# Optimization experiments

Hardware: AMD Instinct MI355X
Metric: run time of the kernel (lower is better)

## Reference

```python
import jax, jax.numpy as jnp
import numpy as np
import math

B, N, D, K = 4, 4096, 1024, 8


def setup_inputs() -> dict:
    key = jax.random.key(0)
    ks = jax.random.split(key, 9)
    s = 0.02
    return {
        "summaries": jax.random.normal(ks[0], (B, N, D), dtype=jnp.float32),
        "Wq": jax.random.normal(ks[1], (D, D), dtype=jnp.float32) * s,
        "bq": jnp.zeros((D,), dtype=jnp.float32),
        "Wk": jax.random.normal(ks[2], (D, D), dtype=jnp.float32) * s,
        "bk": jnp.zeros((D,), dtype=jnp.float32),
        "Wv": jax.random.normal(ks[3], (D, D), dtype=jnp.float32) * s,
        "bv": jnp.zeros((D,), dtype=jnp.float32),
        "Wo": jax.random.normal(ks[4], (D, D), dtype=jnp.float32) * s,
        "bo": jnp.zeros((D,), dtype=jnp.float32),
    }


def reference(summaries, Wq, bq, Wk, bk, Wv, bv, Wo, bo):
    b_, n_, d_ = summaries.shape
    q = summaries @ Wq + bq
    k = summaries @ Wk + bk
    v = summaries @ Wv + bv
    # [B, N, N] causal scores
    scores = jnp.einsum("bnd,bmd->bnm", q, k) / math.sqrt(d_)
    causal = jnp.triu(jnp.full((n_, n_), -jnp.inf, dtype=scores.dtype), k=1)
    scores = scores + causal
    # top-k sparse attention (N > K here, matching the torch branch)
    topk_vals, topk_idx = jax.lax.top_k(scores, K)  # [B, N, K]
    bi = jnp.arange(b_)[:, None, None]
    ri = jnp.arange(n_)[None, :, None]
    sparse = jnp.full_like(scores, -jnp.inf).at[bi, ri, topk_idx].set(topk_vals)
    attn = jax.nn.softmax(sparse, axis=-1)
    out = jnp.einsum("bnm,bmd->bnd", attn, v)
    return out @ Wo + bo
```

## Files before the change

### kernel.cpp

```cpp
#include <hip/hip_runtime.h>
#include <cstdint>
#include <cstddef>

#define B_ 4
#define N_ 4096
#define D_ 1024
#define CAND 16
#define M_ (B_*N_)
#define MD_ ((size_t)M_ * D_)
#define DD_ ((size_t)D_ * D_)

typedef __attribute__((ext_vector_type(8))) short short8;
typedef __attribute__((ext_vector_type(4))) float floatx4;

__device__ __align__(16) float          g_Qf[MD_];
__device__ __align__(16) float          g_Kf[MD_];
__device__ __align__(16) unsigned short g_Qb[MD_];
__device__ __align__(16) unsigned short g_Kb[MD_];
__device__ __align__(16) float          g_Vf[MD_];
__device__ __align__(16) unsigned short g_AO[MD_];
__device__ __align__(16) unsigned short g_X0[MD_];
__device__ __align__(16) unsigned short g_X1[MD_];
__device__ __align__(16) unsigned short g_Wq0T[DD_];
__device__ __align__(16) unsigned short g_Wq1T[DD_];
__device__ __align__(16) unsigned short g_Wk0T[DD_];
__device__ __align__(16) unsigned short g_Wk1T[DD_];
__device__ __align__(16) unsigned short g_WvT[DD_];
__device__ __align__(16) unsigned short g_WoT[DD_];
__device__ __align__(16) float          g_S[(size_t)B_ * N_ * N_];
__device__ __align__(16) int            g_cand[(size_t)M_ * CAND];
__device__ __align__(16) int            g_t8i[(size_t)M_ * 8];
__device__ __align__(16) float          g_t8w[(size_t)M_ * 8];

__device__ __forceinline__ float b2f(unsigned short u){
  return __uint_as_float(((unsigned int)u) << 16);
}
__device__ __forceinline__ unsigned short f2b(float f){
  unsigned int b = __float_as_uint(f);
  b += 0x7fffu + ((b >> 16) & 1u);
  return (unsigned short)(b >> 16);
}
__device__ __forceinline__ void split2(float x, unsigned short& h0,
                                       unsigned short& h1){
  h0 = f2b(x);
  float r1 = x - b2f(h0);
  h1 = f2b(r1);
}

__device__ __forceinline__ void gl_lds16(const void* g, void* l){
  __builtin_amdgcn_global_load_lds(
      (const __attribute__((address_space(1))) unsigned int*)g,
      (__attribute__((address_space(3))) unsigned int*)l, 16, 0, 0);
}

__global__ __launch_bounds__(256)
void transpose2(const float* __restrict__ Wv, const float* __restrict__ Wo){
  __shared__ float tile[32][33];
  const float* src = blockIdx.z ? Wo : Wv;
  unsigned short* dst = blockIdx.z ? g_WoT : g_WvT;
  int tx = threadIdx.x, ty = threadIdx.y;
  int n0 = blockIdx.x * 32, k0 = blockIdx.y * 32;
  for (int r = ty; r < 32; r += 8) tile[r][tx] = src[(size_t)(k0 + r) * D_ + n0 + tx];
  __syncthreads();
  for (int r = ty; r < 32; r += 8) dst[(size_t)(n0 + r) * D_ + k0 + tx] = f2b(tile[tx][r]);
}

__global__ __launch_bounds__(256)
void split_wT(const float* __restrict__ Wq, const float* __restrict__ Wk){
  __shared__ float tile[32][33];
  const float* src = blockIdx.z ? Wk : Wq;
  unsigned short* d0 = blockIdx.z ? g_Wk0T : g_Wq0T;
  unsigned short* d1 = blockIdx.z ? g_Wk1T : g_Wq1T;
  int tx = threadIdx.x, ty = threadIdx.y;
  int n0 = blockIdx.x * 32, k0 = blockIdx.y * 32;
  for (int r = ty; r < 32; r += 8) tile[r][tx] = src[(size_t)(k0 + r) * D_ + n0 + tx];
  __syncthreads();
  for (int r = ty; r < 32; r += 8){
    unsigned short h0, h1;
    split2(tile[tx][r], h0, h1);
    size_t o = (size_t)(n0 + r) * D_ + k0 + tx;
    d0[o] = h0; d1[o] = h1;
  }
}

__global__ __launch_bounds__(256)
void split_x(const float* __restrict__ X){
  size_t i = ((size_t)blockIdx.x * 256 + threadIdx.x) * 4;
  if (i >= MD_) return;
  float4 x = *(const float4*)&X[i];
  ushort4 u0, u1;
  split2(x.x, u0.x, u1.x);
  split2(x.y, u0.y, u1.y);
  split2(x.z, u0.z, u1.z);
  split2(x.w, u0.w, u1.w);
  *(ushort4*)&g_X0[i] = u0;
  *(ushort4*)&g_X1[i] = u1;
}

__global__ __launch_bounds__(256, 2)
void qk_split_gemm(const float* __restrict__ bq, const float* __restrict__ bk){
  int p = blockIdx.x;
  int lin = (p & 7) * 256 + (p >> 3);
  int mt = lin >> 4;
  int sub = lin & 15;
  int which = sub >> 3;
  int nt = sub & 7;

  const unsigned short* __restrict__ B0 = which ? g_Wk0T : g_Wq0T;
  const unsigned short* __restrict__ B1 = which ? g_Wk1T : g_Wq1T;
  const float* __restrict__ bias = which ? bk : bq;
  float* __restrict__ outf = which ? g_Kf : g_Qf;
  unsigned short* __restrict__ outb = which ? g_Kb : g_Qb;

  __shared__ unsigned short __align__(16) As[2][128 * 32];
  __shared__ unsigned short __align__(16) Bs[2][128 * 32];

  int tid = threadIdx.x;
  size_t m0 = (size_t)mt * 128;
  int n0 = nt * 128;
  int l = tid & 63, wid = tid >> 6;
  int wm = (wid >> 1) * 64, wn = (wid & 1) * 64;
  int quad = l >> 4, lr = l & 15;
  int srow = tid >> 2, scol = (tid & 3) * 8;

  floatx4 acc[4][4];
  #pragma unroll
  for (int i = 0; i < 4; i++)
    #pragma unroll
    for (int j = 0; j < 4; j++) acc[i][j] = (floatx4)0.0f;

  for (int k0 = 0; k0 < D_; k0 += 32){
    #pragma unroll
    for (int it2 = 0; it2 < 2; it2++){
      int r = srow + it2 * 64;
      size_t ao = (m0 + r) * D_ + k0 + scol;
      size_t bo = (size_t)(n0 + r) * D_ + k0 + scol;
      int so = r * 32 + scol;
      gl_lds16(&g_X0[ao], &As[0][so]);
      gl_lds16(&g_X1[ao], &As[1][so]);
      gl_lds16(&B0[bo], &Bs[0][so]);
      gl_lds16(&B1[bo], &Bs[1][so]);
    }
    __syncthreads();
    short8 a0[4], a1[4], b0[4], b1[4];
    #pragma unroll
    for (int i = 0; i < 4; i++){
      int ro = (wm + i * 16 + lr) * 32 + quad * 8;
      a0[i] = *(short8*)&As[0][ro];
      a1[i] = *(short8*)&As[1][ro];
    }
    #pragma unroll
    for (int j = 0; j < 4; j++){
      int ro = (wn + j * 16 + lr) * 32 + quad * 8;
      b0[j] = *(short8*)&Bs[0][ro];
      b1[j] = *(short8*)&Bs[1][ro];
    }
    #pragma unroll
    for (int i = 0; i < 4; i++)
      #pragma unroll
      for (int j = 0; j < 4; j++){
        acc[i][j] = __builtin_amdgcn_mfma_f32_16x16x32_bf16(a0[i], b1[j], acc[i][j], 0, 0, 0);
        acc[i][j] = __builtin_amdgcn_mfma_f32_16x16x32_bf16(a1[i], b0[j], acc[i][j], 0, 0, 0);
        acc[i][j] = __builtin_amdgcn_mfma_f32_16x16x32_bf16(a0[i], b0[j], acc[i][j], 0, 0, 0);
      }
    __syncthreads();
  }
  #pragma unroll
  for (int i = 0; i < 4; i++)
    #pragma unroll
    for (int j = 0; j < 4; j++)
      #pragma unroll
      for (int rg = 0; rg < 4; rg++){
        size_t row = m0 + wm + i * 16 + quad * 4 + rg;
        int col = n0 + wn + j * 16 + lr;
        float val = acc[i][j][rg] + bias[col];
        outf[row * D_ + col] = val;
        outb[row * D_ + col] = f2b(val);
      }
}

__global__ __launch_bounds__(256)
void gemm_bf16(const float* __restrict__ bias, float* __restrict__ Cout, int sel){
  const unsigned short* Asrc = sel ? g_AO : g_X0;
  const unsigned short* Bt = sel ? g_WoT : g_WvT;
  float* C = sel ? Cout : g_Vf;
  __shared__ unsigned short __align__(16) As[128 * 32];
  __shared__ unsigned short __align__(16) Bs[128 * 32];
  int p = blockIdx.x;
  int lin = (p & 7) * 128 + (p >> 3);
  int mt = lin >> 3;
  int nt = lin & 7;
  int tid = threadIdx.x;
  size_t m0 = (size_t)mt * 128;
  int n0 = nt * 128;
  int l = tid & 63, wid = tid >> 6;
  int wm = (wid >> 1) * 64, wn = (wid & 1) * 64;
  int quad = l >> 4, lr = l & 15;
  int srow = tid >> 2, scol = (tid & 3) * 8;
  floatx4 acc[4][4];
  #pragma unroll
  for (int i = 0; i < 4; i++)
    #pragma unroll
    for (int j = 0; j < 4; j++) acc[i][j] = (floatx4)0.0f;

  for (int k0 = 0; k0 < D_; k0 += 32){
    #pragma unroll
    for (int it = 0; it < 2; it++){
      int r = srow + it * 64;
      int so = r * 32 + scol;
      gl_lds16(&Asrc[(m0 + r) * D_ + k0 + scol], &As[so]);
      gl_lds16(&Bt[(size_t)(n0 + r) * D_ + k0 + scol], &Bs[so]);
    }
    __syncthreads();
    short8 af[4], bf[4];
    #pragma unroll
    for (int i = 0; i < 4; i++) af[i] = *(short8*)&As[(wm + i * 16 + lr) * 32 + quad * 8];
    #pragma unroll
    for (int j = 0; j < 4; j++) bf[j] = *(short8*)&Bs[(wn + j * 16 + lr) * 32 + quad * 8];
    #pragma unroll
    for (int i = 0; i < 4; i++)
      #pragma unroll
      for (int j = 0; j < 4; j++)
        acc[i][j] = __builtin_amdgcn_mfma_f32_16x16x32_bf16(af[i], bf[j], acc[i][j], 0, 0, 0);
    __syncthreads();
  }
  #pragma unroll
  for (int i = 0; i < 4; i++)
    #pragma unroll
    for (int j = 0; j < 4; j++)
      #pragma unroll
      for (int rg = 0; rg < 4; rg++){
        size_t row = m0 + wm + i * 16 + quad * 4 + rg;
        int col = n0 + wn + j * 16 + lr;
        C[row * D_ + col] = acc[i][j][rg] + bias[col];
      }
}

__global__ __launch_bounds__(256)
void scores_gemm(){
  int jt = blockIdx.x, it = blockIdx.y, b = blockIdx.z;
  if (jt > it) return;
  __shared__ unsigned short __align__(16) As[128 * 32];
  __shared__ unsigned short __align__(16) Bs[128 * 32];
  int tid = threadIdx.x;
  size_t am0 = (size_t)b * N_ + it * 128;
  size_t bn0 = (size_t)b * N_ + jt * 128;
  int l = tid & 63, wid = tid >> 6;
  int wm = (wid >> 1) * 64, wn = (wid & 1) * 64;
  int quad = l >> 4, lr = l & 15;
  int srow = tid >> 2, scol = (tid & 3) * 8;
  floatx4 acc[4][4];
  #pragma unroll
  for (int i = 0; i < 4; i++)
    #pragma unroll
    for (int j = 0; j < 4; j++) acc[i][j] = (floatx4)0.0f;

  for (int k0 = 0; k0 < D_; k0 += 32){
    #pragma unroll
    for (int it2 = 0; it2 < 2; it2++){
      int r = srow + it2 * 64;
      int so = r * 32 + scol;
      gl_lds16(&g_Qb[(am0 + r) * D_ + k0 + scol], &As[so]);
      gl_lds16(&g_Kb[(bn0 + r) * D_ + k0 + scol], &Bs[so]);
    }
    __syncthreads();
    short8 af[4], bf[4];
    #pragma unroll
    for (int i = 0; i < 4; i++) af[i] = *(short8*)&As[(wm + i * 16 + lr) * 32 + quad * 8];
    #pragma unroll
    for (int j = 0; j < 4; j++) bf[j] = *(short8*)&Bs[(wn + j * 16 + lr) * 32 + quad * 8];
    #pragma unroll
    for (int i = 0; i < 4; i++)
      #pragma unroll
      for (int j = 0; j < 4; j++)
        acc[i][j] = __builtin_amdgcn_mfma_f32_16x16x32_bf16(af[i], bf[j], acc[i][j], 0, 0, 0);
    __syncthreads();
  }
  #pragma unroll
  for (int i = 0; i < 4; i++)
    #pragma unroll
    for (int j = 0; j < 4; j++)
      #pragma unroll
      for (int rg = 0; rg < 4; rg++){
        int row = it * 128 + wm + i * 16 + quad * 4 + rg;
        int col = jt * 128 + wn + j * 16 + lr;
        float v = acc[i][j][rg] * 0.03125f;
        if (col > row) v = -3.0e38f;
        g_S[((size_t)b * N_ + row) * N_ + col] = v;
      }
}

__global__ __launch_bounds__(256)
void row_topk(){
  __shared__ float lv[CAND * 256];
  __shared__ int   li[CAND * 256];
  int w = threadIdx.x >> 6, l = threadIdx.x & 63;
  int g = threadIdx.x;
  int i = blockIdx.x * 4 + w;
  int irow = i & (N_ - 1);
  const float* Srow = &g_S[(size_t)i * N_];
  #pragma unroll
  for (int u = 0; u < CAND; u++){ lv[u * 256 + g] = -3.0e38f; li[u * 256 + g] = -1; }
  float vmin = -3.0e38f; int pmin = 0;
  for (int j0 = l * 4; j0 <= irow; j0 += 256){
    float4 v4 = *(const float4*)&Srow[j0];
    #pragma unroll
    for (int e = 0; e < 4; e++){
      float v = (&v4.x)[e];
      if (v > vmin){
        lv[pmin * 256 + g] = v; li[pmin * 256 + g] = j0 + e;
        float m = lv[g]; int p = 0;
        #pragma unroll
        for (int u = 1; u < CAND; u++){ float x = lv[u * 256 + g]; if (x < m){ m = x; p = u; } }
        vmin = m; pmin = p;
      }
    }
  }
  float mv = lv[g]; int mp = 0;
  #pragma unroll
  for (int u = 1; u < CAND; u++){ float x = lv[u * 256 + g]; if (x > mv){ mv = x; mp = u; } }
  int mj = li[mp * 256 + g];
  for (int rd = 0; rd < CAND; rd++){
    float bv = mv; int bj = mj; int bl = l;
    #pragma unroll
    for (int off = 32; off >= 1; off >>= 1){
      float ov = __shfl_xor(bv, off);
      int oj = __shfl_xor(bj, off);
      int ol = __shfl_xor(bl, off);
      if (ov > bv || (ov == bv && ol < bl)){ bv = ov; bj = oj; bl = ol; }
    }
    bool valid = (bv > -2.9e38f);
    if (l == 0) g_cand[(size_t)i * CAND + rd] = valid ? bj : -1;
    if (valid && bl == l){
      lv[mp * 256 + g] = -3.0e38f;
      mv = lv[g]; mp = 0;
      #pragma unroll
      for (int u = 1; u < CAND; u++){ float x = lv[u * 256 + g]; if (x > mv){ mv = x; mp = u; } }
      mj = li[mp * 256 + g];
    }
  }
}

__global__ __launch_bounds__(256)
void rescore_top8(){
  int i = blockIdx.x;
  int b = i >> 12;
  int tid = threadIdx.x, l = tid & 63, w = tid >> 6;
  __shared__ double cs[CAND];
  __shared__ int cid[CAND];
  if (tid < CAND) cid[tid] = g_cand[(size_t)i * CAND + tid];
  __syncthreads();
  double q[16];
  #pragma unroll
  for (int u = 0; u < 16; u++) q[u] = (double)g_Qf[(size_t)i * D_ + l + 64 * u];
  for (int c = w * 4; c < w * 4 + 4; c++){
    int j = cid[c];
    double s = 0.0;
    if (j >= 0){
      size_t ko = ((size_t)(b * N_ + j)) * D_;
      #pragma unroll
      for (int u = 0; u < 16; u++) s = fma(q[u], (double)g_Kf[ko + l + 64 * u], s);
    }
    #pragma unroll
    for (int off = 32; off >= 1; off >>= 1) s += __shfl_down(s, off);
    if (l == 0) cs[c] = (j >= 0) ? s * 0.03125 : -1.0e300;
  }
  __syncthreads();
  if (tid == 0){
    double v8[8]; int i8[8];
    bool used[CAND];
    for (int u = 0; u < CAND; u++) used[u] = false;
    for (int rk = 0; rk < 8; rk++){
      double best = -1.0e300; int bp = -1;
      for (int c = 0; c < CAND; c++)
        if (!used[c] && cid[c] >= 0 && cs[c] > best){ best = cs[c]; bp = c; }
      if (bp >= 0){ used[bp] = true; v8[rk] = best; i8[rk] = cid[bp]; }
      else { v8[rk] = -1.0e300; i8[rk] = -1; }
    }
    if (i8[0] < 0){ i8[0] = i & (N_ - 1); v8[0] = 0.0; }
    double mx = v8[0];
    double e[8]; double Z = 0.0;
    for (int rk = 0; rk < 8; rk++){
      e[rk] = (i8[rk] >= 0) ? exp(v8[rk] - mx) : 0.0;
      Z += e[rk];
    }
    for (int rk = 0; rk < 8; rk++){
      g_t8i[(size_t)i * 8 + rk] = i8[rk];
      g_t8w[(size_t)i * 8 + rk] = (float)(e[rk] / Z);
    }
  }
}

__global__ __launch_bounds__(256)
void gather_v(){
  int i = blockIdx.x;
  int b = i >> 12;
  int tid = threadIdx.x;
  __shared__ float ws8[8];
  __shared__ int id8[8];
  if (tid < 8){ ws8[tid] = g_t8w[(size_t)i * 8 + tid]; id8[tid] = g_t8i[(size_t)i * 8 + tid]; }
  __syncthreads();
  int d0 = tid * 4;
  float a0 = 0.f, a1 = 0.f, a2 = 0.f, a3 = 0.f;
  #pragma unroll
  for (int rk = 0; rk < 8; rk++){
    int j = id8[rk];
    if (j < 0) continue;
    float wgt = ws8[rk];
    float4 vv = *(const float4*)&g_Vf[((size_t)(b * N_ + j)) * D_ + d0];
    a0 += wgt * vv.x; a1 += wgt * vv.y; a2 += wgt * vv.z; a3 += wgt * vv.w;
  }
  ushort4 o;
  o.x = f2b(a0); o.y = f2b(a1); o.z = f2b(a2); o.w = f2b(a3);
  *(ushort4*)&g_AO[(size_t)i * D_ + d0] = o;
}

extern "C" void kernel_launch(void* const* d_in, const int* in_sizes, int n_in,
                              void* d_out, int out_size, void* d_ws, size_t ws_size,
                              hipStream_t stream){
  const float* S  = (const float*)d_in[0];
  const float* Wq = (const float*)d_in[1];
  const float* bq = (const float*)d_in[2];
  const float* Wk = (const float*)d_in[3];
  const float* bk = (const float*)d_in[4];
  const float* Wv = (const float*)d_in[5];
  const float* bv = (const float*)d_in[6];
  const float* Wo = (const float*)d_in[7];
  const float* bo = (const float*)d_in[8];
  float* out = (float*)d_out;
  (void)d_ws; (void)ws_size; (void)in_sizes; (void)n_in; (void)out_size;

  transpose2<<<dim3(32, 32, 2), dim3(32, 8), 0, stream>>>(Wv, Wo);
  split_wT<<<dim3(32, 32, 2), dim3(32, 8), 0, stream>>>(Wq, Wk);
  split_x<<<dim3(M_), 256, 0, stream>>>(S);
  qk_split_gemm<<<dim3(2048), 256, 0, stream>>>(bq, bk);
  gemm_bf16<<<dim3(1024), 256, 0, stream>>>(bv, nullptr, 0);
  scores_gemm<<<dim3(32, 32, 4), 256, 0, stream>>>();
  row_topk<<<dim3(M_ / 4), 256, 0, stream>>>();
  rescore_top8<<<dim3(M_), 256, 0, stream>>>();
  gather_v<<<dim3(M_), 256, 0, stream>>>();
  gemm_bf16<<<dim3(1024), 256, 0, stream>>>(bo, out, 1);
}
```

Before: 1.122 ms.

## Interleave split-bf16 hi/lo operands so Q/K GEMM runs as longer-K single GEMM

```diff
diff --git a/kernel.cpp b/kernel.cpp
--- a/kernel.cpp
+++ b/kernel.cpp
@@ -20,11 +20,11 @@
 __device__ __align__(16) float          g_Vf[MD_];
 __device__ __align__(16) unsigned short g_AO[MD_];
 __device__ __align__(16) unsigned short g_X0[MD_];
-__device__ __align__(16) unsigned short g_X1[MD_];
+__device__ __align__(16) unsigned short g_Xpk[2 * MD_];
 __device__ __align__(16) unsigned short g_Wq0T[DD_];
-__device__ __align__(16) unsigned short g_Wq1T[DD_];
 __device__ __align__(16) unsigned short g_Wk0T[DD_];
-__device__ __align__(16) unsigned short g_Wk1T[DD_];
+__device__ __align__(16) unsigned short g_Wqpk[2 * DD_];
+__device__ __align__(16) unsigned short g_Wkpk[2 * DD_];
 __device__ __align__(16) unsigned short g_WvT[DD_];
 __device__ __align__(16) unsigned short g_WoT[DD_];
 __device__ __align__(16) float          g_S[(size_t)B_ * N_ * N_];
@@ -69,8 +69,8 @@
 void split_wT(const float* __restrict__ Wq, const float* __restrict__ Wk){
   __shared__ float tile[32][33];
   const float* src = blockIdx.z ? Wk : Wq;
-  unsigned short* d0 = blockIdx.z ? g_Wk0T : g_Wq0T;
-  unsigned short* d1 = blockIdx.z ? g_Wk1T : g_Wq1T;
+  unsigned short* d0  = blockIdx.z ? g_Wk0T : g_Wq0T;
+  unsigned short* dpk = blockIdx.z ? g_Wkpk : g_Wqpk;
   int tx = threadIdx.x, ty = threadIdx.y;
   int n0 = blockIdx.x * 32, k0 = blockIdx.y * 32;
   for (int r = ty; r < 32; r += 8) tile[r][tx] = src[(size_t)(k0 + r) * D_ + n0 + tx];
@@ -79,7 +79,9 @@
     unsigned short h0, h1;
     split2(tile[tx][r], h0, h1);
     size_t o = (size_t)(n0 + r) * D_ + k0 + tx;
-    d0[o] = h0; d1[o] = h1;
+    d0[o] = h0;
+    *(unsigned int*)&dpk[(size_t)(n0 + r) * (2 * D_) + 2 * (k0 + tx)] =
+        (unsigned int)h1 | ((unsigned int)h0 << 16);
   }
 }
 
@@ -88,17 +90,19 @@
   size_t i = ((size_t)blockIdx.x * 256 + threadIdx.x) * 4;
   if (i >= MD_) return;
   float4 x = *(const float4*)&X[i];
-  ushort4 u0, u1;
-  split2(x.x, u0.x, u1.x);
-  split2(x.y, u0.y, u1.y);
-  split2(x.z, u0.z, u1.z);
-  split2(x.w, u0.w, u1.w);
+  ushort4 u0;
+  uint4 pk;
+  unsigned short h0, h1;
+  split2(x.x, h0, h1); u0.x = h0; pk.x = (unsigned int)h0 | ((unsigned int)h1 << 16);
+  split2(x.y, h0, h1); u0.y = h0; pk.y = (unsigned int)h0 | ((unsigned int)h1 << 16);
+  split2(x.z, h0, h1); u0.z = h0; pk.z = (unsigned int)h0 | ((unsigned int)h1 << 16);
+  split2(x.w, h0, h1); u0.w = h0; pk.w = (unsigned int)h0 | ((unsigned int)h1 << 16);
   *(ushort4*)&g_X0[i] = u0;
-  *(ushort4*)&g_X1[i] = u1;
+  *(uint4*)&g_Xpk[2 * i] = pk;
 }
 
 __global__ __launch_bounds__(256, 2)
-void qk_split_gemm(const float* __restrict__ bq, const float* __restrict__ bk){
+void qk_pack_gemm(const float* __restrict__ bq, const float* __restrict__ bk){
   int p = blockIdx.x;
   int lin = (p & 7) * 256 + (p >> 3);
   int mt = lin >> 4;
@@ -106,14 +110,14 @@
   int which = sub >> 3;
   int nt = sub & 7;
 
-  const unsigned short* __restrict__ B0 = which ? g_Wk0T : g_Wq0T;
-  const unsigned short* __restrict__ B1 = which ? g_Wk1T : g_Wq1T;
+  const unsigned short* __restrict__ Bpk = which ? g_Wkpk : g_Wqpk;
+  const unsigned short* __restrict__ B0  = which ? g_Wk0T : g_Wq0T;
   const float* __restrict__ bias = which ? bk : bq;
   float* __restrict__ outf = which ? g_Kf : g_Qf;
   unsigned short* __restrict__ outb = which ? g_Kb : g_Qb;
 
-  __shared__ unsigned short __align__(16) As[2][128 * 32];
-  __shared__ unsigned short __align__(16) Bs[2][128 * 32];
+  __shared__ unsigned short __align__(16) As[128 * 32];
+  __shared__ unsigned short __align__(16) Bs[128 * 32];
 
   int tid = threadIdx.x;
   size_t m0 = (size_t)mt * 128;
@@ -129,40 +133,46 @@
     #pragma unroll
     for (int j = 0; j < 4; j++) acc[i][j] = (floatx4)0.0f;
 
-  for (int k0 = 0; k0 < D_; k0 += 32){
+  for (int k0 = 0; k0 < 2 * D_; k0 += 32){
     #pragma unroll
     for (int it2 = 0; it2 < 2; it2++){
       int r = srow + it2 * 64;
-      size_t ao = (m0 + r) * D_ + k0 + scol;
-      size_t bo = (size_t)(n0 + r) * D_ + k0 + scol;
       int so = r * 32 + scol;
-      gl_lds16(&g_X0[ao], &As[0][so]);
-      gl_lds16(&g_X1[ao], &As[1][so]);
-      gl_lds16(&B0[bo], &Bs[0][so]);
-      gl_lds16(&B1[bo], &Bs[1][so]);
-    }
-    __syncthreads();
-    short8 a0[4], a1[4], b0[4], b1[4];
-    #pragma unroll
-    for (int i = 0; i < 4; i++){
-      int ro = (wm + i * 16 + lr) * 32 + quad * 8;
-      a0[i] = *(short8*)&As[0][ro];
-      a1[i] = *(short8*)&As[1][ro];
-    }
-    #pragma unroll
-    for (int j = 0; j < 4; j++){
-      int ro = (wn + j * 16 + lr) * 32 + quad * 8;
-      b0[j] = *(short8*)&Bs[0][ro];
-      b1[j] = *(short8*)&Bs[1][ro];
-    }
+      gl_lds16(&g_Xpk[(m0 + r) * (2 * D_) + k0 + scol], &As[so]);
+      gl_lds16(&Bpk[(size_t)(n0 + r) * (2 * D_) + k0 + scol], &Bs[so]);
+    }
+    __syncthreads();
+    short8 af[4], bf[4];
+    #pragma unroll
+    for (int i = 0; i < 4; i++) af[i] = *(short8*)&As[(wm + i * 16 + lr) * 32 + quad * 8];
+    #pragma unroll
+    for (int j = 0; j < 4; j++) bf[j] = *(short8*)&Bs[(wn + j * 16 + lr) * 32 + quad * 8];
     #pragma unroll
     for (int i = 0; i < 4; i++)
       #pragma unroll
-      for (int j = 0; j < 4; j++){
-        acc[i][j] = __builtin_amdgcn_mfma_f32_16x16x32_bf16(a0[i], b1[j], acc[i][j], 0, 0, 0);
-        acc[i][j] = __builtin_amdgcn_mfma_f32_16x16x32_bf16(a1[i], b0[j], acc[i][j], 0, 0, 0);
-        acc[i][j] = __builtin_amdgcn_mfma_f32_16x16x32_bf16(a0[i], b0[j], acc[i][j], 0, 0, 0);
-      }
+      for (int j = 0; j < 4; j++)
+        acc[i][j] = __builtin_amdgcn_mfma_f32_16x16x32_bf16(af[i], bf[j], acc[i][j], 0, 0, 0);
+    __syncthreads();
+  }
+  for (int k0 = 0; k0 < D_; k0 += 32){
+    #pragma unroll
+    for (int it2 = 0; it2 < 2; it2++){
+      int r = srow + it2 * 64;
+      int so = r * 32 + scol;
+      gl_lds16(&g_X0[(m0 + r) * D_ + k0 + scol], &As[so]);
+      gl_lds16(&B0[(size_t)(n0 + r) * D_ + k0 + scol], &Bs[so]);
+    }
+    __syncthreads();
+    short8 af[4], bf[4];
+    #pragma unroll
+    for (int i = 0; i < 4; i++) af[i] = *(short8*)&As[(wm + i * 16 + lr) * 32 + quad * 8];
+    #pragma unroll
+    for (int j = 0; j < 4; j++) bf[j] = *(short8*)&Bs[(wn + j * 16 + lr) * 32 + quad * 8];
+    #pragma unroll
+    for (int i = 0; i < 4; i++)
+      #pragma unroll
+      for (int j = 0; j < 4; j++)
+        acc[i][j] = __builtin_amdgcn_mfma_f32_16x16x32_bf16(af[i], bf[j], acc[i][j], 0, 0, 0);
     __syncthreads();
   }
   #pragma unroll
@@ -433,7 +443,7 @@
   transpose2<<<dim3(32, 32, 2), dim3(32, 8), 0, stream>>>(Wv, Wo);
   split_wT<<<dim3(32, 32, 2), dim3(32, 8), 0, stream>>>(Wq, Wk);
   split_x<<<dim3(M_), 256, 0, stream>>>(S);
-  qk_split_gemm<<<dim3(2048), 256, 0, stream>>>(bq, bk);
+  qk_pack_gemm<<<dim3(2048), 256, 0, stream>>>(bq, bk);
   gemm_bf16<<<dim3(1024), 256, 0, stream>>>(bv, nullptr, 0);
   scores_gemm<<<dim3(32, 32, 4), 256, 0, stream>>>();
   row_topk<<<dim3(M_ / 4), 256, 0, stream>>>();
```

After: 1.228 ms. +9.4%, slower.
